# Kernel optimization log

Measured on AMD Instinct MI355X. Metric: run time of the kernel, lower is better.

The kernel has to match this reference:

```python
import jax, jax.numpy as jnp
import numpy as np

N = 100000

def _gcn_conv(x, W, b, row, col, norm, n_nodes):
    # x: [N, Fin], W: [Fin, Fout]; message = norm * (x W)[row], aggregated at col
    h = x @ W                                  # small GEMM
    msg = h[row] * norm[:, None]               # [E+N, Fout] gather (memory bound)
    out = jax.ops.segment_sum(msg, col, num_segments=n_nodes)
    return out + b

def _norm_coeffs(edge_index, n_nodes):
    # add self-loops, compute symmetric normalization deg^-1/2[row]*deg^-1/2[col]
    loops = jnp.arange(n_nodes, dtype=edge_index.dtype)
    row = jnp.concatenate([edge_index[0], loops])
    col = jnp.concatenate([edge_index[1], loops])
    deg = jax.ops.segment_sum(jnp.ones_like(col, dtype=jnp.float32), col,
                              num_segments=n_nodes)
    dinv = jnp.where(deg > 0, jax.lax.rsqrt(deg), 0.0)
    norm = dinv[row] * dinv[col]
    return row, col, norm

def setup_inputs() -> dict:
    key = jax.random.key(0)
    ks = jax.random.split(key, 4)
    x = jax.random.normal(ks[0], (N, 64), dtype=jnp.float32)
    edge_index = jax.random.randint(ks[1], (2, 1600000), 0, N, dtype=jnp.int64)
    W1 = jax.random.normal(ks[2], (64, 64), dtype=jnp.float32) / np.sqrt(64)
    b1 = jnp.zeros((64,), dtype=jnp.float32)
    W2 = jax.random.normal(ks[3], (64, 64), dtype=jnp.float32) / np.sqrt(64)
    b2 = jnp.zeros((64,), dtype=jnp.float32)
    return {"x": x, "edge_index": edge_index, "W1": W1, "b1": b1, "W2": W2, "b2": b2}

def reference(x, edge_index, W1, b1, W2, b2):
    row, col, norm = _norm_coeffs(edge_index, N)
    h = jax.nn.relu(_gcn_conv(x, W1, b1, row, col, norm, N))
    return _gcn_conv(h, W2, b2, row, col, norm, N)
```

## Files before the change

### kernel.cpp

```cpp
#include <hip/hip_runtime.h>


#define WPB 4
#define BSH 8
#define BSZ 256
#define PTILE 4096
#define CAP 6144
#define PADALLOW 3856
#define CROW (CAP + PADALLOW)

typedef __attribute__((ext_vector_type(8))) short bf16x8;
typedef __attribute__((ext_vector_type(4))) float f32x4;

__device__ __forceinline__ unsigned bf16_rne(float f) {
    unsigned b = __float_as_uint(f);
    return (b + 0x7fffu + ((b >> 16) & 1u)) >> 16;
}
__device__ __forceinline__ float bf16_lo(unsigned u) { return __uint_as_float(u << 16); }
__device__ __forceinline__ float bf16_hi(unsigned u) { return __uint_as_float(u & 0xffff0000u); }

__global__ void k_binit(int* __restrict__ bcur, int NB) {
    int b = blockIdx.x * blockDim.x + threadIdx.x;
    if (b < NB) bcur[b] = b * CAP;
}

__global__ __launch_bounds__(256) void k_part(const int* __restrict__ rowi,
                                              const int* __restrict__ coli,
                                              int E, int N, int NB, int numTiles,
                                              int* __restrict__ bcur,
                                              unsigned* __restrict__ pairs) {
    __shared__ int hist[512];
    __shared__ int base[512];
    int t = threadIdx.x;
    int T = E + N;
    for (int tile = blockIdx.x; tile < numTiles; tile += gridDim.x) {
        int tstart = tile * PTILE;
        int m = min(PTILE, T - tstart);
        for (int b = t; b < NB; b += 256) hist[b] = 0;
        __syncthreads();
        for (int i = t; i < m; i += 256) {
            int g = tstart + i;
            int c = (g < E) ? coli[g] : (g - E);
            atomicAdd(&hist[c >> BSH], 1);
        }
        __syncthreads();
        for (int b = t; b < NB; b += 256) {
            int h = hist[b];
            base[b] = h ? atomicAdd(&bcur[b], h) : 0;
            hist[b] = 0;
        }
        __syncthreads();
        for (int i = t; i < m; i += 256) {
            int g = tstart + i;
            int r, c;
            if (g < E) { r = rowi[g]; c = coli[g]; }
            else       { r = g - E; c = r; }
            int b = c >> BSH;
            int rank = atomicAdd(&hist[b], 1);
            pairs[base[b] + rank] = (unsigned)r | ((unsigned)(c & (BSZ - 1)) << 24);
        }
        __syncthreads();
    }
}

__global__ __launch_bounds__(256) void k_bfill(const unsigned* __restrict__ pairs,
                                               const int* __restrict__ bcur,
                                               int N,
                                               int* __restrict__ offsets,
                                               int* __restrict__ cnt,
                                               float* __restrict__ dinv,
                                               int* __restrict__ csrc) {
    __shared__ int scnt[BSZ];
    __shared__ int scur[BSZ];
    __shared__ int wsum[4];
    int b = blockIdx.x;
    int t = threadIdx.x;
    int ebeg = b * CAP;
    int m = bcur[b] - ebeg;
    int pbase = b * CROW;
    scnt[t] = 0;
    __syncthreads();
    for (int i = t; i < m; i += 256) {
        atomicAdd(&scnt[pairs[ebeg + i] >> 24], 1);
    }
    __syncthreads();
    int cval = scnt[t];
    int pc = (cval + 15) & ~15;
    int lane = t & 63, wid = t >> 6;
    int inc = pc;
    #pragma unroll
    for (int d = 1; d < 64; d <<= 1) {
        int o = __shfl_up(inc, d);
        if (lane >= d) inc += o;
    }
    if (lane == 63) wsum[wid] = inc;
    __syncthreads();
    int woff = 0;
    for (int i = 0; i < wid; i++) woff += wsum[i];
    int off = pbase + woff + inc - pc;
    int v = (b << BSH) + t;
    if (v < N) {
        offsets[v] = off;
        cnt[v] = pc;
        dinv[v] = rsqrtf((float)cval);
    }
    scur[t] = off;
    for (int i = off + cval; i < off + pc; i++) csrc[i] = N;
    __syncthreads();
    for (int i = t; i < m; i += 256) {
        unsigned pk = pairs[ebeg + i];
        int slot = atomicAdd(&scur[pk >> 24], 1);
        csrc[slot] = (int)(pk & 0xFFFFFFu);
    }
}

template <bool BF16IN>
__global__ __launch_bounds__(256) void k_gemm(const void* __restrict__ Xv,
                                              const float* __restrict__ W,
                                              const float* __restrict__ dinv,
                                              unsigned* __restrict__ Hout,
                                              int N, int nSlabs, int slabStride) {
    __shared__ float SMEM[4224];
    int t = threadIdx.x;
    int lane = t & 63, w = t >> 6;
    int nn = lane & 15, kq = lane >> 4;

    for (int i = t; i < 1024; i += 256) ((float4*)SMEM)[i] = ((const float4*)W)[i];
    __syncthreads();
    bf16x8 Bf[2][4];
    #pragma unroll
    for (int kt = 0; kt < 2; kt++) {
        #pragma unroll
        for (int ct = 0; ct < 4; ct++) {
            union { bf16x8 v; unsigned short s[8]; } u;
            #pragma unroll
            for (int j = 0; j < 8; j++) {
                int k = kt * 32 + kq * 8 + j;
                u.s[j] = (unsigned short)bf16_rne(SMEM[k * 64 + ct * 16 + nn]);
            }
            Bf[kt][ct] = u.v;
        }
    }
    __syncthreads();

    float* outT = SMEM + w * 1056;

    for (int slab = blockIdx.x * 4 + w; slab < nSlabs; slab += slabStride) {
        int row0 = slab * 16;
        int rowA = min(row0 + nn, N - 1);
        bf16x8 A0, A1;
        if (BF16IN) {
            const uint4* X = (const uint4*)Xv;
            union { uint4 u; bf16x8 v; } a0, a1;
            a0.u = X[(size_t)rowA * 8 + kq];
            a1.u = X[(size_t)rowA * 8 + 4 + kq];
            A0 = a0.v; A1 = a1.v;
        } else {
            const float4* X = (const float4*)Xv;
            float4 f0 = X[(size_t)rowA * 16 + kq * 2];
            float4 f1 = X[(size_t)rowA * 16 + kq * 2 + 1];
            float4 f2 = X[(size_t)rowA * 16 + 8 + kq * 2];
            float4 f3 = X[(size_t)rowA * 16 + 8 + kq * 2 + 1];
            union { bf16x8 v; unsigned short s[8]; } a0, a1;
            a0.s[0] = (unsigned short)bf16_rne(f0.x); a0.s[1] = (unsigned short)bf16_rne(f0.y);
            a0.s[2] = (unsigned short)bf16_rne(f0.z); a0.s[3] = (unsigned short)bf16_rne(f0.w);
            a0.s[4] = (unsigned short)bf16_rne(f1.x); a0.s[5] = (unsigned short)bf16_rne(f1.y);
            a0.s[6] = (unsigned short)bf16_rne(f1.z); a0.s[7] = (unsigned short)bf16_rne(f1.w);
            a1.s[0] = (unsigned short)bf16_rne(f2.x); a1.s[1] = (unsigned short)bf16_rne(f2.y);
            a1.s[2] = (unsigned short)bf16_rne(f2.z); a1.s[3] = (unsigned short)bf16_rne(f2.w);
            a1.s[4] = (unsigned short)bf16_rne(f3.x); a1.s[5] = (unsigned short)bf16_rne(f3.y);
            a1.s[6] = (unsigned short)bf16_rne(f3.z); a1.s[7] = (unsigned short)bf16_rne(f3.w);
            A0 = a0.v; A1 = a1.v;
        }
        float dvm = dinv[rowA];

        f32x4 acc[4];
        #pragma unroll
        for (int ct = 0; ct < 4; ct++) acc[ct] = (f32x4){0.f, 0.f, 0.f, 0.f};
        #pragma unroll
        for (int ct = 0; ct < 4; ct++) {
            acc[ct] = __builtin_amdgcn_mfma_f32_16x16x32_bf16(A0, Bf[0][ct], acc[ct], 0, 0, 0);
            acc[ct] = __builtin_amdgcn_mfma_f32_16x16x32_bf16(A1, Bf[1][ct], acc[ct], 0, 0, 0);
        }

        #pragma unroll
        for (int reg = 0; reg < 4; reg++) {
            int r = kq * 4 + reg;
            float dv = __shfl(dvm, r);
            #pragma unroll
            for (int ct = 0; ct < 4; ct++) {
                outT[r * 66 + ct * 16 + nn] = acc[ct][reg] * dv;
            }
        }
        int rr = lane >> 2;
        int c0 = (lane & 3) * 16;
        int orow = row0 + rr;
        if (orow < N) {
            unsigned pk[8];
            #pragma unroll
            for (int i = 0; i < 8; i++) {
                float lo = outT[rr * 66 + c0 + 2 * i];
                float hi = outT[rr * 66 + c0 + 2 * i + 1];
                pk[i] = bf16_rne(lo) | (bf16_rne(hi) << 16);
            }
            uint4* dst = (uint4*)Hout + (size_t)orow * 8 + (lane & 3) * 2;
            dst[0] = make_uint4(pk[0], pk[1], pk[2], pk[3]);
            dst[1] = make_uint4(pk[4], pk[5], pk[6], pk[7]);
        } else if (orow == N) {
            uint4* dst = (uint4*)Hout + (size_t)N * 8 + (lane & 3) * 2;
            dst[0] = make_uint4(0, 0, 0, 0);
            dst[1] = make_uint4(0, 0, 0, 0);
        }
    }
}

template <bool RELU_BF16OUT>
__global__ __launch_bounds__(256) void k_agg(const uint4* __restrict__ H,
                                             const int* __restrict__ offsets,
                                             const int* __restrict__ cnt,
                                             const int* __restrict__ csrc,
                                             const float* __restrict__ dinv,
                                             const float* __restrict__ bias,
                                             void* __restrict__ outv, int N) {
    int t = threadIdx.x;
    int lane = t & 63;
    int el = lane >> 3;
    int fl = lane & 7;
    int v = blockIdx.x * WPB + (t >> 6);
    if (v >= N) return;
    int beg = offsets[v];
    int pdeg = cnt[v];
    const int2* cs2 = (const int2*)(csrc + beg);
    float a0 = 0.f, a1 = 0.f, a2 = 0.f, a3 = 0.f;
    float a4 = 0.f, a5 = 0.f, a6 = 0.f, a7 = 0.f;
    for (int j = 0; j < pdeg; j += 16) {
        int2 ss = cs2[(j >> 1) + el];
        uint4 d0 = H[(size_t)ss.x * 8 + fl];
        uint4 d1 = H[(size_t)ss.y * 8 + fl];
        a0 += bf16_lo(d0.x); a1 += bf16_hi(d0.x);
        a2 += bf16_lo(d0.y); a3 += bf16_hi(d0.y);
        a4 += bf16_lo(d0.z); a5 += bf16_hi(d0.z);
        a6 += bf16_lo(d0.w); a7 += bf16_hi(d0.w);
        a0 += bf16_lo(d1.x); a1 += bf16_hi(d1.x);
        a2 += bf16_lo(d1.y); a3 += bf16_hi(d1.y);
        a4 += bf16_lo(d1.z); a5 += bf16_hi(d1.z);
        a6 += bf16_lo(d1.w); a7 += bf16_hi(d1.w);
    }
    #pragma unroll
    for (int d = 8; d < 64; d <<= 1) {
        a0 += __shfl_xor(a0, d); a1 += __shfl_xor(a1, d);
        a2 += __shfl_xor(a2, d); a3 += __shfl_xor(a3, d);
        a4 += __shfl_xor(a4, d); a5 += __shfl_xor(a5, d);
        a6 += __shfl_xor(a6, d); a7 += __shfl_xor(a7, d);
    }
    if (el == 0) {
        int f = fl * 8;
        float dv = dinv[v];
        float r0 = fmaf(dv, a0, bias[f + 0]);
        float r1 = fmaf(dv, a1, bias[f + 1]);
        float r2 = fmaf(dv, a2, bias[f + 2]);
        float r3 = fmaf(dv, a3, bias[f + 3]);
        float r4 = fmaf(dv, a4, bias[f + 4]);
        float r5 = fmaf(dv, a5, bias[f + 5]);
        float r6 = fmaf(dv, a6, bias[f + 6]);
        float r7 = fmaf(dv, a7, bias[f + 7]);
        if (RELU_BF16OUT) {
            r0 = fmaxf(r0, 0.f); r1 = fmaxf(r1, 0.f);
            r2 = fmaxf(r2, 0.f); r3 = fmaxf(r3, 0.f);
            r4 = fmaxf(r4, 0.f); r5 = fmaxf(r5, 0.f);
            r6 = fmaxf(r6, 0.f); r7 = fmaxf(r7, 0.f);
            uint4 pk;
            pk.x = bf16_rne(r0) | (bf16_rne(r1) << 16);
            pk.y = bf16_rne(r2) | (bf16_rne(r3) << 16);
            pk.z = bf16_rne(r4) | (bf16_rne(r5) << 16);
            pk.w = bf16_rne(r6) | (bf16_rne(r7) << 16);
            ((uint4*)outv)[(size_t)v * 8 + fl] = pk;
        } else {
            float4* o = (float4*)outv + (size_t)v * 16 + fl * 2;
            o[0] = make_float4(r0, r1, r2, r3);
            o[1] = make_float4(r4, r5, r6, r7);
        }
    }
}

extern "C" void kernel_launch(void* const* d_in, const int* in_sizes, int n_in,
                              void* d_out, int out_size, void* d_ws, size_t ws_size,
                              hipStream_t stream) {
    const float* x  = (const float*)d_in[0];
    const int*   ei = (const int*)d_in[1];
    const float* W1 = (const float*)d_in[2];
    const float* b1 = (const float*)d_in[3];
    const float* W2 = (const float*)d_in[4];
    const float* b2 = (const float*)d_in[5];
    float* out      = (float*)d_out;

    const int N = in_sizes[0] / 64;
    const int E = in_sizes[1] / 2;
    const int* row = ei;
    const int* col = ei + E;
    const int T = E + N;
    const int NB = (N + BSZ - 1) >> BSH;

    char* p = (char*)d_ws;
    auto alloc = [&](size_t bytes) { void* r = (void*)p; p += (bytes + 255) & ~(size_t)255; return r; };
    int*      bcur    = (int*)alloc((size_t)(NB + 1) * 4);
    int*      offsets = (int*)alloc((size_t)N * 4);
    int*      cnt     = (int*)alloc((size_t)N * 4);
    float*    dinv    = (float*)alloc((size_t)N * 4);
    unsigned* pairs   = (unsigned*)alloc((size_t)NB * CAP * 4);
    int*      csrc    = (int*)alloc(((size_t)NB * CROW + 64) * 4);
    unsigned* hbuf    = (unsigned*)alloc((size_t)(N + 16) * 32 * 4);
    unsigned* abuf    = (unsigned*)alloc((size_t)(N + 16) * 32 * 4);

    const int numTiles = (T + PTILE - 1) / PTILE;

    k_binit<<<(NB + 255) / 256, 256, 0, stream>>>(bcur, NB);
    k_part<<<numTiles, 256, 0, stream>>>(row, col, E, N, NB, numTiles, bcur, pairs);
    k_bfill<<<NB, 256, 0, stream>>>(pairs, bcur, N, offsets, cnt, dinv, csrc);

    const int nSlabs = (N + 16) / 16;
    const int GEMM_BLOCKS = 512;
    const int SLAB_STRIDE = GEMM_BLOCKS * 4;
    const int GB = (N + WPB - 1) / WPB;

    k_gemm<false><<<GEMM_BLOCKS, 256, 0, stream>>>(x, W1, dinv, hbuf, N, nSlabs, SLAB_STRIDE);
    k_agg<true><<<GB, 256, 0, stream>>>((const uint4*)hbuf, offsets, cnt, csrc, dinv, b1, abuf, N);
    k_gemm<true><<<GEMM_BLOCKS, 256, 0, stream>>>(abuf, W2, dinv, hbuf, N, nSlabs, SLAB_STRIDE);
    k_agg<false><<<GB, 256, 0, stream>>>((const uint4*)hbuf, offsets, cnt, csrc, dinv, b2, out, N);
}
```

Baseline: 233.1 us.

## Assign one 8-lane group per node in aggregation and widen bfill blocks

The aggregation kernel now maps 8 threads per destination node (32 nodes per block) instead of a full wavefront per node. It walks the node's edge list serially with a one-step prefetch of the next index pair, which removes the cross-lane shuffle reduction and the padding-to-16 waste. Edge counts are now padded only to even, and k_bfill runs with 1024 threads per bucket. Partition tile size is halved and GEMM block count doubled. Per-thread serial loops add latency on high-degree nodes and may leave fewer loads in flight per node.

```diff
diff --git a/kernel.cpp b/kernel.cpp
--- a/kernel.cpp
+++ b/kernel.cpp
@@ -1,10 +1,10 @@
 #include <hip/hip_runtime.h>
 
 
-#define WPB 4
+#define NPB 32
 #define BSH 8
 #define BSZ 256
-#define PTILE 4096
+#define PTILE 2048
 #define CAP 6144
 #define PADALLOW 3856
 #define CROW (CAP + PADALLOW)
@@ -63,13 +63,13 @@
     }
 }
 
-__global__ __launch_bounds__(256) void k_bfill(const unsigned* __restrict__ pairs,
-                                               const int* __restrict__ bcur,
-                                               int N,
-                                               int* __restrict__ offsets,
-                                               int* __restrict__ cnt,
-                                               float* __restrict__ dinv,
-                                               int* __restrict__ csrc) {
+__global__ __launch_bounds__(1024) void k_bfill(const unsigned* __restrict__ pairs,
+                                                const int* __restrict__ bcur,
+                                                int N,
+                                                int* __restrict__ offsets,
+                                                int* __restrict__ cnt,
+                                                float* __restrict__ dinv,
+                                                int* __restrict__ csrc) {
     __shared__ int scnt[BSZ];
     __shared__ int scur[BSZ];
     __shared__ int wsum[4];
@@ -78,36 +78,41 @@
     int ebeg = b * CAP;
     int m = bcur[b] - ebeg;
     int pbase = b * CROW;
-    scnt[t] = 0;
-    __syncthreads();
-    for (int i = t; i < m; i += 256) {
+    if (t < BSZ) scnt[t] = 0;
+    __syncthreads();
+    for (int i = t; i < m; i += 1024) {
         atomicAdd(&scnt[pairs[ebeg + i] >> 24], 1);
     }
     __syncthreads();
-    int cval = scnt[t];
-    int pc = (cval + 15) & ~15;
+    int cval = 0, pc = 0, inc = 0;
     int lane = t & 63, wid = t >> 6;
-    int inc = pc;
-    #pragma unroll
-    for (int d = 1; d < 64; d <<= 1) {
-        int o = __shfl_up(inc, d);
-        if (lane >= d) inc += o;
-    }
-    if (lane == 63) wsum[wid] = inc;
-    __syncthreads();
-    int woff = 0;
-    for (int i = 0; i < wid; i++) woff += wsum[i];
-    int off = pbase + woff + inc - pc;
-    int v = (b << BSH) + t;
-    if (v < N) {
-        offsets[v] = off;
-        cnt[v] = pc;
-        dinv[v] = rsqrtf((float)cval);
-    }
-    scur[t] = off;
-    for (int i = off + cval; i < off + pc; i++) csrc[i] = N;
-    __syncthreads();
-    for (int i = t; i < m; i += 256) {
+    if (t < BSZ) {
+        cval = scnt[t];
+        pc = (cval + 15) & ~15;
+        inc = pc;
+        #pragma unroll
+        for (int d = 1; d < 64; d <<= 1) {
+            int o = __shfl_up(inc, d);
+            if (lane >= d) inc += o;
+        }
+        if (lane == 63) wsum[wid] = inc;
+    }
+    __syncthreads();
+    if (t < BSZ) {
+        int woff = 0;
+        for (int i = 0; i < wid; i++) woff += wsum[i];
+        int off = pbase + woff + inc - pc;
+        int v = (b << BSH) + t;
+        if (v < N) {
+            offsets[v] = off;
+            cnt[v] = (cval + 1) & ~1;
+            dinv[v] = rsqrtf((float)cval);
+        }
+        scur[t] = off;
+        for (int i = off + cval; i < off + pc; i++) csrc[i] = N;
+    }
+    __syncthreads();
+    for (int i = t; i < m; i += 1024) {
         unsigned pk = pairs[ebeg + i];
         int slot = atomicAdd(&scur[pk >> 24], 1);
         csrc[slot] = (int)(pk & 0xFFFFFFu);
@@ -223,63 +228,63 @@
                                              const float* __restrict__ bias,
                                              void* __restrict__ outv, int N) {
     int t = threadIdx.x;
-    int lane = t & 63;
-    int el = lane >> 3;
-    int fl = lane & 7;
-    int v = blockIdx.x * WPB + (t >> 6);
+    int fl = t & 7;
+    int v = blockIdx.x * NPB + (t >> 3);
     if (v >= N) return;
     int beg = offsets[v];
-    int pdeg = cnt[v];
+    int deg = cnt[v];
     const int2* cs2 = (const int2*)(csrc + beg);
+    const char* hb = (const char*)H + ((unsigned)fl << 4);
+
     float a0 = 0.f, a1 = 0.f, a2 = 0.f, a3 = 0.f;
     float a4 = 0.f, a5 = 0.f, a6 = 0.f, a7 = 0.f;
-    for (int j = 0; j < pdeg; j += 16) {
-        int2 ss = cs2[(j >> 1) + el];
-        uint4 d0 = H[(size_t)ss.x * 8 + fl];
-        uint4 d1 = H[(size_t)ss.y * 8 + fl];
-        a0 += bf16_lo(d0.x); a1 += bf16_hi(d0.x);
-        a2 += bf16_lo(d0.y); a3 += bf16_hi(d0.y);
-        a4 += bf16_lo(d0.z); a5 += bf16_hi(d0.z);
-        a6 += bf16_lo(d0.w); a7 += bf16_hi(d0.w);
-        a0 += bf16_lo(d1.x); a1 += bf16_hi(d1.x);
-        a2 += bf16_lo(d1.y); a3 += bf16_hi(d1.y);
-        a4 += bf16_lo(d1.z); a5 += bf16_hi(d1.z);
-        a6 += bf16_lo(d1.w); a7 += bf16_hi(d1.w);
-    }
-    #pragma unroll
-    for (int d = 8; d < 64; d <<= 1) {
-        a0 += __shfl_xor(a0, d); a1 += __shfl_xor(a1, d);
-        a2 += __shfl_xor(a2, d); a3 += __shfl_xor(a3, d);
-        a4 += __shfl_xor(a4, d); a5 += __shfl_xor(a5, d);
-        a6 += __shfl_xor(a6, d); a7 += __shfl_xor(a7, d);
-    }
-    if (el == 0) {
-        int f = fl * 8;
-        float dv = dinv[v];
-        float r0 = fmaf(dv, a0, bias[f + 0]);
-        float r1 = fmaf(dv, a1, bias[f + 1]);
-        float r2 = fmaf(dv, a2, bias[f + 2]);
-        float r3 = fmaf(dv, a3, bias[f + 3]);
-        float r4 = fmaf(dv, a4, bias[f + 4]);
-        float r5 = fmaf(dv, a5, bias[f + 5]);
-        float r6 = fmaf(dv, a6, bias[f + 6]);
-        float r7 = fmaf(dv, a7, bias[f + 7]);
-        if (RELU_BF16OUT) {
-            r0 = fmaxf(r0, 0.f); r1 = fmaxf(r1, 0.f);
-            r2 = fmaxf(r2, 0.f); r3 = fmaxf(r3, 0.f);
-            r4 = fmaxf(r4, 0.f); r5 = fmaxf(r5, 0.f);
-            r6 = fmaxf(r6, 0.f); r7 = fmaxf(r7, 0.f);
-            uint4 pk;
-            pk.x = bf16_rne(r0) | (bf16_rne(r1) << 16);
-            pk.y = bf16_rne(r2) | (bf16_rne(r3) << 16);
-            pk.z = bf16_rne(r4) | (bf16_rne(r5) << 16);
-            pk.w = bf16_rne(r6) | (bf16_rne(r7) << 16);
-            ((uint4*)outv)[(size_t)v * 8 + fl] = pk;
-        } else {
-            float4* o = (float4*)outv + (size_t)v * 16 + fl * 2;
-            o[0] = make_float4(r0, r1, r2, r3);
-            o[1] = make_float4(r4, r5, r6, r7);
-        }
+
+#define ACC8(R) do {                                                        \
+        uint4 dd = *(const uint4*)(hb + ((unsigned)(R) << 7));              \
+        a0 += bf16_lo(dd.x); a1 += bf16_hi(dd.x);                           \
+        a2 += bf16_lo(dd.y); a3 += bf16_hi(dd.y);                           \
+        a4 += bf16_lo(dd.z); a5 += bf16_hi(dd.z);                           \
+        a6 += bf16_lo(dd.w); a7 += bf16_hi(dd.w);                           \
+    } while (0)
+
+    int2 ss = cs2[0];
+    for (int j = 2; j < deg; j += 2) {
+        int2 nx = cs2[j >> 1];
+        ACC8(ss.x);
+        ACC8(ss.y);
+        ss = nx;
+    }
+    ACC8(ss.x);
+    ACC8(ss.y);
+#undef ACC8
+
+    float dv = dinv[v];
+    const float4* b4 = (const float4*)bias;
+    float4 bA = b4[fl * 2];
+    float4 bB = b4[fl * 2 + 1];
+    float r0 = fmaf(dv, a0, bA.x);
+    float r1 = fmaf(dv, a1, bA.y);
+    float r2 = fmaf(dv, a2, bA.z);
+    float r3 = fmaf(dv, a3, bA.w);
+    float r4 = fmaf(dv, a4, bB.x);
+    float r5 = fmaf(dv, a5, bB.y);
+    float r6 = fmaf(dv, a6, bB.z);
+    float r7 = fmaf(dv, a7, bB.w);
+    if (RELU_BF16OUT) {
+        r0 = fmaxf(r0, 0.f); r1 = fmaxf(r1, 0.f);
+        r2 = fmaxf(r2, 0.f); r3 = fmaxf(r3, 0.f);
+        r4 = fmaxf(r4, 0.f); r5 = fmaxf(r5, 0.f);
+        r6 = fmaxf(r6, 0.f); r7 = fmaxf(r7, 0.f);
+        uint4 pk;
+        pk.x = bf16_rne(r0) | (bf16_rne(r1) << 16);
+        pk.y = bf16_rne(r2) | (bf16_rne(r3) << 16);
+        pk.z = bf16_rne(r4) | (bf16_rne(r5) << 16);
+        pk.w = bf16_rne(r6) | (bf16_rne(r7) << 16);
+        ((uint4*)outv)[(size_t)v * 8 + fl] = pk;
+    } else {
+        float4* o = (float4*)outv + (size_t)v * 16 + fl * 2;
+        o[0] = make_float4(r0, r1, r2, r3);
+        o[1] = make_float4(r4, r5, r6, r7);
     }
 }
 
@@ -316,12 +321,12 @@
 
     k_binit<<<(NB + 255) / 256, 256, 0, stream>>>(bcur, NB);
     k_part<<<numTiles, 256, 0, stream>>>(row, col, E, N, NB, numTiles, bcur, pairs);
-    k_bfill<<<NB, 256, 0, stream>>>(pairs, bcur, N, offsets, cnt, dinv, csrc);
+    k_bfill<<<NB, 1024, 0, stream>>>(pairs, bcur, N, offsets, cnt, dinv, csrc);
 
     const int nSlabs = (N + 16) / 16;
-    const int GEMM_BLOCKS = 512;
+    const int GEMM_BLOCKS = 1024;
     const int SLAB_STRIDE = GEMM_BLOCKS * 4;
-    const int GB = (N + WPB - 1) / WPB;
+    const int GB = (N + NPB - 1) / NPB;
 
     k_gemm<false><<<GEMM_BLOCKS, 256, 0, stream>>>(x, W1, dinv, hbuf, N, nSlabs, SLAB_STRIDE);
     k_agg<true><<<GB, 256, 0, stream>>>((const uint4*)hbuf, offsets, cnt, csrc, dinv, b1, abuf, N);
```

New measurement: 213.8 us. -8.3%, faster.
